# Performance work log

Measured on AMD Instinct MI355X. Metric: run time of the kernel, lower is better.

## Reference

```python
import jax, jax.numpy as jnp
import numpy as np

D_MODEL = 1024
N_HEADS = 16
HEAD_DIM = D_MODEL // N_HEADS  # 64
BUCKET = 64


def setup_inputs() -> dict:
    key = jax.random.key(0)
    k1, k2, k3 = jax.random.split(key, 3)
    B, T = 4, 4096
    x = jax.random.normal(k1, (B, T, D_MODEL), dtype=jnp.float32)
    # torch nn.Linear(d, 3d, bias=False): weight shape (3d, d), y = x @ W.T
    W_qkv = jax.random.normal(k2, (3 * D_MODEL, D_MODEL), dtype=jnp.float32) * (D_MODEL ** -0.5)
    W_out = jax.random.normal(k3, (D_MODEL, D_MODEL), dtype=jnp.float32) * (D_MODEL ** -0.5)
    return {"x": x, "W_qkv": W_qkv, "W_out": W_out}


def reference(x, W_qkv, W_out):
    B, T, _ = x.shape
    qkv = x @ W_qkv.T                                  # [B, T, 3*d_model]
    # split_heads with Hs=head_dim -> [B, 3*nH, T, Hs]; chunk along head axis
    qkv = qkv.reshape(B, T, 3 * N_HEADS, HEAD_DIM).transpose(0, 2, 1, 3)
    q, k, v = jnp.split(qkv, 3, axis=1)                # each [B, nH, T, Hs]

    q = jax.nn.softmax(q, axis=-1) * (HEAD_DIM ** -0.5)
    k = jnp.exp(k)                                     # causal path (mask is None)

    n = T // BUCKET
    bucket = lambda t: t.reshape(B, N_HEADS, n, BUCKET, HEAD_DIM)
    b_q, b_k, b_v = bucket(q), bucket(k), bucket(v)    # [B, H, n, s, d]

    # per-bucket key sums, inclusive cumsum over buckets, then shift to exclusive
    b_k_sum = jnp.sum(b_k, axis=-2)                    # [B, H, n, d]
    b_k_cumsum = jnp.cumsum(b_k_sum, axis=-2)
    b_k_cumsum = jnp.pad(b_k_cumsum, ((0, 0), (0, 0), (1, 0), (0, 0)))[:, :, :-1]

    # per-bucket kv outer products, exclusive cumsum over buckets
    context = jnp.einsum('bhnsd,bhnse->bhnde', b_k, b_v)        # [B, H, n, d, e]
    context = jnp.cumsum(context, axis=-3)
    context = jnp.pad(context, ((0, 0), (0, 0), (1, 0), (0, 0), (0, 0)))[:, :, :-1]

    den = jnp.einsum('bhnsd,bhnd->bhns', b_q, b_k_cumsum)
    D_inv = 1.0 / jnp.maximum(den, 1e-6)
    attn = jnp.einsum('bhnsd,bhnde,bhns->bhnse', b_q, context, D_inv)

    xo = attn.reshape(B, N_HEADS, T, HEAD_DIM)         # [B, H, T, Hs]
    xo = xo.transpose(0, 2, 1, 3).reshape(B, T, D_MODEL)  # cat_heads
    return xo @ W_out.T
```

## Files before the change

kernel.cpp:

```cpp
#include <hip/hip_runtime.h>
#include <hip/hip_bf16.h>
#include <math.h>

typedef __hip_bfloat16 bf16;
typedef __attribute__((ext_vector_type(4))) float f32x4;
typedef __attribute__((ext_vector_type(8))) short bf16x8s;

#define T_SEQ 4096
#define MFMA16(a, b, c) __builtin_amdgcn_mfma_f32_16x16x32_bf16(a, b, c, 0, 0, 0)
#define AS1 __attribute__((address_space(1)))
#define AS3 __attribute__((address_space(3)))

static __device__ __forceinline__ float bf2f(short u) {
    return __uint_as_float(((unsigned int)(unsigned short)u) << 16);
}
static __device__ __forceinline__ short f2bf(float f) {
    bf16 h = __float2bfloat16(f);
    union { bf16 b; short s; } c; c.b = h; return c.s;
}
static __device__ __forceinline__ int swz_f(int r) { return (r & 7) ^ (r >> 3); }

__global__ void cvt_f32_bf16(const float* __restrict__ src, bf16* __restrict__ dst, int n8) {
    int i = blockIdx.x * 256 + threadIdx.x;
    if (i >= n8) return;
    f32x4 a = ((const f32x4*)src)[(size_t)i * 2];
    f32x4 b = ((const f32x4*)src)[(size_t)i * 2 + 1];
    union { bf16 h[8]; uint4 u; } p;
    p.h[0] = __float2bfloat16(a.x); p.h[1] = __float2bfloat16(a.y);
    p.h[2] = __float2bfloat16(a.z); p.h[3] = __float2bfloat16(a.w);
    p.h[4] = __float2bfloat16(b.x); p.h[5] = __float2bfloat16(b.y);
    p.h[6] = __float2bfloat16(b.z); p.h[7] = __float2bfloat16(b.w);
    ((uint4*)dst)[i] = p.u;
}

template<int MODE>
__global__ __launch_bounds__(512, 2)
void gemm256(const bf16* __restrict__ A, const bf16* __restrict__ Bm,
             int K, int N,
             bf16* __restrict__ out0, bf16* __restrict__ ctxb, float* __restrict__ ksum,
             float* __restrict__ outf)
{
    __shared__ __align__(16) short SMEM[65536];
    const int tid  = threadIdx.x;
    const int l    = tid & 63;
    const int wid  = tid >> 6;
    const int wr   = wid >> 2;
    const int wc   = wid & 3;

    const int nwg  = gridDim.x * gridDim.y;
    const int flat = blockIdx.y * gridDim.x + blockIdx.x;
    const int swzb = (flat & 7) * (nwg >> 3) + (flat >> 3);
    const int bx   = swzb % gridDim.x;
    const int by   = swzb / gridDim.x;
    const int brow = by * 256;
    const int bcol = bx * 256;
    const int nkt  = K >> 6;

    const bool isKV = (MODE == 0) && (bx >= 4);
    const int  jkv  = bx - 4;
    const int  b0row = isKV ? (1024 + jkv * 128) : bcol;
    const int  b1row = isKV ? (2048 + jkv * 128) : bcol + 128;

    const int chnk = (l >> 4) ^ (((l & 15) >> 1) & 3);
    const short* baseA = &SMEM[(wr * 128 + (l & 15)) * 32 + chnk * 8];
    const short* baseB = &SMEM[32768 + (wc * 64 + (l & 15)) * 32 + chnk * 8];
#define RDA(BUF, KH, M_) (*(const bf16x8s*)(baseA + (BUF) * 16384 + (KH) * 8192 + (M_) * 512))
#define RDB(BUF, KH, N_) (*(const bf16x8s*)(baseB + (BUF) * 16384 + (KH) * 8192 + (N_) * 512))

    const int srow = tid >> 2;
    const int scs  = (tid & 3) ^ ((srow >> 1) & 3);
    const bf16* gA0 = A  + (size_t)(brow + srow) * K + scs * 8;
    const bf16* gA1 = A  + (size_t)(brow + 128 + srow) * K + scs * 8;
    const bf16* gB0 = Bm + (size_t)(b0row + srow) * K + scs * 8;
    const bf16* gB1 = Bm + (size_t)(b1row + srow) * K + scs * 8;
#define GLL(PTR, KH, BUF, ISB, EXTRA)                                             \
    __builtin_amdgcn_global_load_lds((const AS1 void*)((PTR) + (KH) * 32),        \
        (AS3 void*)&SMEM[(ISB) * 32768 + ((BUF) * 2 + (KH)) * 8192 + (EXTRA) + tid * 8], 16, 0, 0)

    f32x4 acc[8][4];
#pragma unroll
    for (int m = 0; m < 8; ++m)
#pragma unroll
        for (int n = 0; n < 4; ++n) acc[m][n] = (f32x4){0.f, 0.f, 0.f, 0.f};

    GLL(gA0, 0, 0, 0, 0);    GLL(gA1, 0, 0, 0, 4096);
    GLL(gB0, 0, 0, 1, 0);    GLL(gB1, 0, 0, 1, 4096);
    GLL(gA0, 1, 0, 0, 0);    GLL(gA1, 1, 0, 0, 4096);
    GLL(gB0, 1, 0, 1, 0);    GLL(gB1, 1, 0, 1, 4096);

    const bf16 *pA0 = gA0 + 64, *pA1 = gA1 + 64, *pB0 = gB0 + 64, *pB1 = gB1 + 64;

#define PHASE(CUR, NXT, KS, PF)                                                   \
    {                                                                             \
        bf16x8s afr[8], bfr[4];                                                   \
        if (PF) { asm volatile("s_waitcnt vmcnt(4)" ::: "memory"); }              \
        else    { asm volatile("s_waitcnt vmcnt(0)" ::: "memory"); }              \
        __builtin_amdgcn_s_barrier();                                             \
        __builtin_amdgcn_sched_barrier(0);                                        \
        _Pragma("unroll") for (int n = 0; n < 4; ++n) bfr[n] = RDB(CUR, KS, n);   \
        _Pragma("unroll") for (int m = 0; m < 8; ++m) afr[m] = RDA(CUR, KS, m);   \
        if (PF) { GLL(pA0, KS, NXT, 0, 0); GLL(pA1, KS, NXT, 0, 4096);            \
                  GLL(pB0, KS, NXT, 1, 0); GLL(pB1, KS, NXT, 1, 4096); }          \
        __builtin_amdgcn_s_setprio(1);                                            \
        _Pragma("unroll")                                                         \
        for (int m = 0; m < 8; ++m)                                               \
            _Pragma("unroll")                                                     \
            for (int n = 0; n < 4; ++n)                                           \
                acc[m][n] = MFMA16(afr[m], bfr[n], acc[m][n]);                    \
        __builtin_amdgcn_s_setprio(0);                                            \
        __builtin_amdgcn_s_barrier();                                             \
    }

#define BODY(CUR, NXT, TT)                                                        \
    {                                                                             \
        const bool pf = ((TT) + 1 < nkt);                                         \
        PHASE(CUR, NXT, 0, pf)                                                    \
        PHASE(CUR, NXT, 1, pf)                                                    \
        pA0 += 64; pA1 += 64; pB0 += 64; pB1 += 64;                               \
    }

    for (int t = 0; t < nkt; t += 2) {
        BODY(0, 1, t)
        BODY(1, 0, t + 1)
    }

    if (MODE == 1) {
#pragma unroll
        for (int m = 0; m < 8; ++m) {
            int row = brow + wr * 128 + m * 16 + ((l >> 4) << 2);
#pragma unroll
            for (int n = 0; n < 4; ++n) {
                int col = bcol + wc * 64 + n * 16 + (l & 15);
#pragma unroll
                for (int r = 0; r < 4; ++r)
                    outf[(size_t)(row + r) * N + col] = acc[m][n][r];
            }
        }
    } else if (!isKV) {
#pragma unroll
        for (int m = 0; m < 8; ++m) {
            int row = brow + wr * 128 + m * 16 + ((l >> 4) << 2);
#pragma unroll
            for (int r = 0; r < 4; ++r) {
                float v0 = acc[m][0][r], v1 = acc[m][1][r], v2 = acc[m][2][r], v3 = acc[m][3][r];
                float mx = fmaxf(fmaxf(v0, v1), fmaxf(v2, v3));
#pragma unroll
                for (int off = 8; off; off >>= 1) mx = fmaxf(mx, __shfl_xor(mx, off));
                float e0 = __expf(v0 - mx), e1 = __expf(v1 - mx);
                float e2 = __expf(v2 - mx), e3 = __expf(v3 - mx);
                float sm = e0 + e1 + e2 + e3;
#pragma unroll
                for (int off = 8; off; off >>= 1) sm += __shfl_xor(sm, off);
                float inv = 0.125f / sm;
                size_t rr = (size_t)(row + r);
                int cb = bcol + wc * 64 + (l & 15);
                out0[rr * 1024 + cb]      = __float2bfloat16(e0 * inv);
                out0[rr * 1024 + cb + 16] = __float2bfloat16(e1 * inv);
                out0[rr * 1024 + cb + 32] = __float2bfloat16(e2 * inv);
                out0[rr * 1024 + cb + 48] = __float2bfloat16(e3 * inv);
            }
        }
    } else {
        const int hl = wc & 1;
        short* side = (short*)SMEM + ((wc >= 2) ? 32768 : 0);
        float ks[2][4];
#pragma unroll
        for (int u = 0; u < 2; ++u)
#pragma unroll
            for (int n = 0; n < 4; ++n) ks[u][n] = 0.f;
#pragma unroll
        for (int m = 0; m < 8; ++m) {
            const int ubase = wr * 16384 + (m >> 2) * 8192 + hl * 4096;
            const int s0 = (m & 3) * 16 + ((l >> 4) << 2);
            const int sc = s0 >> 3, slo = s0 & 7;
#pragma unroll
            for (int n = 0; n < 4; ++n) {
                int d = n * 16 + (l & 15);
                union { short h4[4]; uint2 u2; } pk;
                if (wc < 2) {
                    float e0 = __expf(acc[m][n][0]), e1 = __expf(acc[m][n][1]);
                    float e2 = __expf(acc[m][n][2]), e3 = __expf(acc[m][n][3]);
                    ks[m >> 2][n] += (e0 + e1) + (e2 + e3);
                    pk.h4[0] = f2bf(e0); pk.h4[1] = f2bf(e1);
                    pk.h4[2] = f2bf(e2); pk.h4[3] = f2bf(e3);
                } else {
                    pk.h4[0] = f2bf(acc[m][n][0]); pk.h4[1] = f2bf(acc[m][n][1]);
                    pk.h4[2] = f2bf(acc[m][n][2]); pk.h4[3] = f2bf(acc[m][n][3]);
                }
                *(uint2*)&side[ubase + d * 64 + ((sc ^ swz_f(d)) << 3) + slo] = pk.u2;
            }
        }
        if (wc < 2) {
#pragma unroll
            for (int u = 0; u < 2; ++u)
#pragma unroll
                for (int n = 0; n < 4; ++n) {
                    float s = ks[u][n];
                    s += __shfl_xor(s, 16);
                    s += __shfl_xor(s, 32);
                    if ((l >> 4) == 0) {
                        int unit = wr * 4 + u * 2 + hl;
                        int gr0 = brow + (unit >> 1) * 64;
                        size_t bidu = (size_t)(((gr0 >> 12) * 16) + jkv * 2 + (unit & 1)) * 64
                                      + ((gr0 & 4095) >> 6);
                        ksum[bidu * 64 + n * 16 + (l & 15)] = s;
                    }
                }
        }
        __syncthreads();

        const int gr0 = brow + (wid >> 1) * 64;
        const size_t bid = (size_t)(((gr0 >> 12) * 16) + jkv * 2 + (wid & 1)) * 64
                           + ((gr0 & 4095) >> 6);
        const short* k_u = (const short*)SMEM + wid * 4096;
        const short* v_u = (const short*)SMEM + 32768 + wid * 4096;

        f32x4 a16[4][4];
#pragma unroll
        for (int m = 0; m < 4; ++m)
#pragma unroll
            for (int n = 0; n < 4; ++n) a16[m][n] = (f32x4){0.f, 0.f, 0.f, 0.f};
#pragma unroll
        for (int kk = 0; kk < 2; ++kk) {
            const int cc = kk * 4 + (l >> 4);
            bf16x8s af[4], bf[4];
#pragma unroll
            for (int m = 0; m < 4; ++m) {
                int rA = m * 16 + (l & 15);
                af[m] = *(const bf16x8s*)&k_u[rA * 64 + ((cc ^ swz_f(rA)) << 3)];
                bf[m] = *(const bf16x8s*)&v_u[rA * 64 + ((cc ^ swz_f(rA)) << 3)];
            }
#pragma unroll
            for (int m = 0; m < 4; ++m)
#pragma unroll
                for (int n = 0; n < 4; ++n)
                    a16[m][n] = MFMA16(af[m], bf[n], a16[m][n]);
        }
        bf16* rec = ctxb + bid * 4096;
#pragma unroll
        for (int m = 0; m < 4; ++m) {
            int d0 = m * 16 + ((l >> 4) << 2);
#pragma unroll
            for (int n = 0; n < 4; ++n) {
                int e = n * 16 + (l & 15);
                ushort4 o;
                o.x = (ushort)f2bf(a16[m][n][0]); o.y = (ushort)f2bf(a16[m][n][1]);
                o.z = (ushort)f2bf(a16[m][n][2]); o.w = (ushort)f2bf(a16[m][n][3]);
                *(ushort4*)&rec[e * 64 + d0] = o;
            }
        }
    }
#undef RDA
#undef RDB
#undef GLL
#undef PHASE
#undef BODY
}

__global__ void cumsum_excl(const bf16* __restrict__ ctxb, const float* __restrict__ ksum,
                            bf16* __restrict__ ctp, float* __restrict__ ksump)
{
    const int bh = blockIdx.y;
    if (blockIdx.x == 4) {
        int d = threadIdx.x;
        if (d >= 64) return;
        float run = 0.f;
        for (int j = 0; j < 64; ++j) {
            size_t idx = (size_t)(bh * 64 + j) * 64 + d;
            float v = ksum[idx];
            ksump[idx] = run;
            run += v;
        }
        return;
    }
    int e0 = (blockIdx.x * 256 + threadIdx.x) * 4;
    float r0 = 0.f, r1 = 0.f, r2 = 0.f, r3 = 0.f;
    for (int j = 0; j < 64; ++j) {
        size_t idx = (size_t)(bh * 64 + j) * 4096 + e0;
        ushort4 v = *(const ushort4*)&ctxb[idx];
        ushort4 o;
        o.x = (ushort)f2bf(r0); o.y = (ushort)f2bf(r1);
        o.z = (ushort)f2bf(r2); o.w = (ushort)f2bf(r3);
        *(ushort4*)&ctp[idx] = o;
        r0 += bf2f((short)v.x); r1 += bf2f((short)v.y);
        r2 += bf2f((short)v.z); r3 += bf2f((short)v.w);
    }
}

__global__ __launch_bounds__(256)
void bucket_attn(const bf16* __restrict__ Qb, const bf16* __restrict__ ctp,
                 const float* __restrict__ ksump, bf16* __restrict__ attn)
{
    __shared__ __align__(16) short q_bf[64 * 64];
    __shared__ __align__(16) short ct_bf[64 * 64];
    __shared__ __align__(16) short at_s[64 * 72];
    __shared__ float dinv_s[64];
    __shared__ float ksum_s[64];
    const int bid = blockIdx.x;
    const int bh = bid >> 6, n = bid & 63;
    const int b = bh >> 4, h = bh & 15;
    const size_t rowbase = (size_t)(b * T_SEQ + n * 64) * 1024 + h * 64;
    const int tid = threadIdx.x;
    const int l = tid & 63, w = tid >> 6;

#pragma unroll
    for (int j = 0; j < 2; ++j) {
        int i = tid + 256 * j;
        int e = i >> 3, dc = i & 7;
        bf16x8s cv = *(const bf16x8s*)&ctp[(size_t)bid * 4096 + e * 64 + dc * 8];
        *(bf16x8s*)&ct_bf[e * 64 + ((dc ^ swz_f(e)) << 3)] = cv;
    }
    if (tid < 64) ksum_s[tid] = ksump[(size_t)bid * 64 + tid];
    __syncthreads();

#pragma unroll
    for (int i = 0; i < 16; ++i) {
        int s = w * 16 + i;
        float qv = bf2f(*(const short*)&Qb[rowbase + (size_t)s * 1024 + l]);
        float dp = qv * ksum_s[l];
#pragma unroll
        for (int off = 32; off; off >>= 1) dp += __shfl_xor(dp, off);
        if (l == 0) dinv_s[s] = 1.f / fmaxf(dp, 1e-6f);
        q_bf[s * 64 + ((((l >> 3)) ^ swz_f(s)) << 3) + (l & 7)] = f2bf(qv);
    }
    __syncthreads();

    f32x4 acc[4];
#pragma unroll
    for (int i = 0; i < 4; ++i) acc[i] = (f32x4){0.f, 0.f, 0.f, 0.f};
    bf16x8s afr[2], bfr[2][4];
#pragma unroll
    for (int kk = 0; kk < 2; ++kk) {
        int cc = kk * 4 + (l >> 4);
        int r = w * 16 + (l & 15);
        afr[kk] = *(const bf16x8s*)&q_bf[r * 64 + ((cc ^ swz_f(r)) << 3)];
#pragma unroll
        for (int n4 = 0; n4 < 4; ++n4) {
            int e = n4 * 16 + (l & 15);
            bfr[kk][n4] = *(const bf16x8s*)&ct_bf[e * 64 + ((cc ^ swz_f(e)) << 3)];
        }
    }
#pragma unroll
    for (int kk = 0; kk < 2; ++kk)
#pragma unroll
        for (int n4 = 0; n4 < 4; ++n4)
            acc[n4] = MFMA16(afr[kk], bfr[kk][n4], acc[n4]);

#pragma unroll
    for (int n4 = 0; n4 < 4; ++n4) {
        int e = n4 * 16 + (l & 15);
#pragma unroll
        for (int r = 0; r < 4; ++r) {
            int s = w * 16 + ((l >> 4) << 2) + r;
            at_s[s * 72 + e] = f2bf(acc[n4][r] * dinv_s[s]);
        }
    }
    __syncthreads();

#pragma unroll
    for (int j = 0; j < 2; ++j) {
        int i = tid + 256 * j;
        int s = i >> 3, c = i & 7;
        bf16x8s v = *(const bf16x8s*)&at_s[s * 72 + c * 8];
        *(bf16x8s*)&attn[rowbase + (size_t)s * 1024 + c * 8] = v;
    }
}

extern "C" void kernel_launch(void* const* d_in, const int* in_sizes, int n_in,
                              void* d_out, int out_size, void* d_ws, size_t ws_size,
                              hipStream_t stream)
{
    const float* x    = (const float*)d_in[0];
    const float* Wqkv = (const float*)d_in[1];
    const float* Wout = (const float*)d_in[2];

    char* ws = (char*)d_ws;
    size_t off = 0;
    auto alloc = [&](size_t bytes) { void* p = ws + off; off += (bytes + 255) & ~(size_t)255; return p; };
    bf16*  xb    = (bf16*)alloc((size_t)16384 * 1024 * 2);
    bf16*  wqkvb = (bf16*)alloc((size_t)3072 * 1024 * 2);
    bf16*  woutb = (bf16*)alloc((size_t)1024 * 1024 * 2);
    bf16*  Qb    = (bf16*)alloc((size_t)16384 * 1024 * 2);
    bf16*  ctxb  = (bf16*)alloc((size_t)4096 * 4096 * 2);
    float* ksum  = (float*)alloc((size_t)4096 * 64 * 4);
    bf16*  ctp   = (bf16*)alloc((size_t)4096 * 4096 * 2);
    float* ksump = (float*)alloc((size_t)4096 * 64 * 4);
    bf16*  attnb = xb;
    float* outf  = (float*)d_out;

    cvt_f32_bf16<<<dim3(16384 * 1024 / 8 / 256), 256, 0, stream>>>(x, xb, 16384 * 1024 / 8);
    cvt_f32_bf16<<<dim3(3072 * 1024 / 8 / 256), 256, 0, stream>>>(Wqkv, wqkvb, 3072 * 1024 / 8);
    cvt_f32_bf16<<<dim3(1024 * 1024 / 8 / 256), 256, 0, stream>>>(Wout, woutb, 1024 * 1024 / 8);

    gemm256<0><<<dim3(12, 64), 512, 0, stream>>>(xb, wqkvb, 1024, 3072, Qb, ctxb, ksum, nullptr);
    cumsum_excl<<<dim3(5, 64), 256, 0, stream>>>(ctxb, ksum, ctp, ksump);
    bucket_attn<<<dim3(4096), 256, 0, stream>>>(Qb, ctp, ksump, attnb);
    gemm256<1><<<dim3(4, 64), 512, 0, stream>>>(attnb, woutb, 1024, 1024, nullptr, nullptr, nullptr, outf);
}
```

Baseline: 239.6 us.

## Interleave GEMM LDS reads, prefetch issues and MFMA in finer half-tile stages

Restructures the GEMM main loop so each k-half is split into two MFMA blocks of four A fragments. Fragment reads and global-to-LDS prefetches are spread between the blocks, and waits use a fixed vmcnt. The aim is to overlap LDS reads and global loads with MFMA more finely and to hold fewer A fragments in registers. It adds more barriers, and the fixed vmcnt(4) with no drain in the last iteration may be incorrect for synchronisation.

New measurement: 232.4 us. -3.0%, faster.

```diff
diff --git a/kernel.cpp b/kernel.cpp
--- a/kernel.cpp
+++ b/kernel.cpp
@@ -87,35 +87,42 @@
     GLL(gB0, 0, 0, 1, 0);    GLL(gB1, 0, 0, 1, 4096);
     GLL(gA0, 1, 0, 0, 0);    GLL(gA1, 1, 0, 0, 4096);
     GLL(gB0, 1, 0, 1, 0);    GLL(gB1, 1, 0, 1, 4096);
+    asm volatile("s_waitcnt vmcnt(4)" ::: "memory");
+    __builtin_amdgcn_s_barrier();
 
     const bf16 *pA0 = gA0 + 64, *pA1 = gA1 + 64, *pB0 = gB0 + 64, *pB1 = gB1 + 64;
 
-#define PHASE(CUR, NXT, KS, PF)                                                   \
-    {                                                                             \
-        bf16x8s afr[8], bfr[4];                                                   \
-        if (PF) { asm volatile("s_waitcnt vmcnt(4)" ::: "memory"); }              \
-        else    { asm volatile("s_waitcnt vmcnt(0)" ::: "memory"); }              \
-        __builtin_amdgcn_s_barrier();                                             \
-        __builtin_amdgcn_sched_barrier(0);                                        \
-        _Pragma("unroll") for (int n = 0; n < 4; ++n) bfr[n] = RDB(CUR, KS, n);   \
-        _Pragma("unroll") for (int m = 0; m < 8; ++m) afr[m] = RDA(CUR, KS, m);   \
-        if (PF) { GLL(pA0, KS, NXT, 0, 0); GLL(pA1, KS, NXT, 0, 4096);            \
-                  GLL(pB0, KS, NXT, 1, 0); GLL(pB1, KS, NXT, 1, 4096); }          \
-        __builtin_amdgcn_s_setprio(1);                                            \
+#define MFMA_BLOCK(ACCOFF)                                                        \
+    __builtin_amdgcn_s_barrier();                                                 \
+    __builtin_amdgcn_s_setprio(1);                                                \
+    _Pragma("unroll")                                                             \
+    for (int m = 0; m < 4; ++m)                                                   \
         _Pragma("unroll")                                                         \
-        for (int m = 0; m < 8; ++m)                                               \
-            _Pragma("unroll")                                                     \
-            for (int n = 0; n < 4; ++n)                                           \
-                acc[m][n] = MFMA16(afr[m], bfr[n], acc[m][n]);                    \
-        __builtin_amdgcn_s_setprio(0);                                            \
-        __builtin_amdgcn_s_barrier();                                             \
-    }
+        for (int n = 0; n < 4; ++n)                                               \
+            acc[m + (ACCOFF)][n] = MFMA16(afr[m], bfr[n], acc[m + (ACCOFF)][n]);  \
+    __builtin_amdgcn_s_setprio(0);                                                \
+    __builtin_amdgcn_s_barrier();
 
 #define BODY(CUR, NXT, TT)                                                        \
     {                                                                             \
         const bool pf = ((TT) + 1 < nkt);                                         \
-        PHASE(CUR, NXT, 0, pf)                                                    \
-        PHASE(CUR, NXT, 1, pf)                                                    \
+        bf16x8s afr[4], bfr[4];                                                   \
+        _Pragma("unroll") for (int n = 0; n < 4; ++n) bfr[n] = RDB(CUR, 0, n);    \
+        _Pragma("unroll") for (int m = 0; m < 4; ++m) afr[m] = RDA(CUR, 0, m);    \
+        if (pf) { GLL(pA0, 0, NXT, 0, 0); GLL(pA1, 0, NXT, 0, 4096); }            \
+        MFMA_BLOCK(0)                                                             \
+        _Pragma("unroll") for (int m = 0; m < 4; ++m) afr[m] = RDA(CUR, 0, m + 4);\
+        if (pf) { GLL(pB0, 0, NXT, 1, 0); GLL(pB1, 0, NXT, 1, 4096); }            \
+        asm volatile("s_waitcnt vmcnt(4)" ::: "memory");                          \
+        MFMA_BLOCK(4)                                                             \
+        _Pragma("unroll") for (int n = 0; n < 4; ++n) bfr[n] = RDB(CUR, 1, n);    \
+        _Pragma("unroll") for (int m = 0; m < 4; ++m) afr[m] = RDA(CUR, 1, m);    \
+        if (pf) { GLL(pA0, 1, NXT, 0, 0); GLL(pA1, 1, NXT, 0, 4096); }            \
+        MFMA_BLOCK(0)                                                             \
+        _Pragma("unroll") for (int m = 0; m < 4; ++m) afr[m] = RDA(CUR, 1, m + 4);\
+        if (pf) { GLL(pB0, 1, NXT, 1, 0); GLL(pB1, 1, NXT, 1, 4096); }            \
+        asm volatile("s_waitcnt vmcnt(4)" ::: "memory");                          \
+        MFMA_BLOCK(4)                                                             \
         pA0 += 64; pA1 += 64; pB0 += 64; pB1 += 64;                               \
     }
 
@@ -253,7 +260,7 @@
 #undef RDA
 #undef RDB
 #undef GLL
-#undef PHASE
+#undef MFMA_BLOCK
 #undef BODY
 }
 
```
